# Kernel optimization log

Hardware: AMD Instinct MI355X
Metric: run time of the kernel (lower is better)

## Reference

```python
import jax, jax.numpy as jnp
import numpy as np

K = 5  # AUTKC top-K parameter


def setup_inputs() -> dict:
    key = jax.random.key(0)
    k1, k2 = jax.random.split(key)
    B, C = 4096, 32000
    pred = jax.random.normal(k1, (B, C), dtype=jnp.float32)
    y = jax.random.randint(k2, (B,), 0, C, dtype=jnp.int64)
    return {"pred": pred, "y": y, "epoch": 1}


def reference(pred, y, epoch):
    # epoch >= epoch_to_paced (=0), so the main AUTKC branch runs.
    B, C = pred.shape
    # surrogate != 'Hinge' -> softmax over classes
    probs = jax.nn.softmax(pred, axis=-1)                      # [B, C]
    pred_p = probs[jnp.arange(B), y][:, None]                  # [B, 1] positive-class prob
    pos_mask = jnp.arange(C)[None, :] == y[:, None]            # [B, C] boolean one-hot
    # Mask out the positive entry; top_k(K+1) over negatives == sort desc + take K+1.
    neg = jnp.where(pos_mask, -jnp.inf, probs)                 # [B, C]
    top_n, _ = jax.lax.top_k(neg, K + 1)                       # [B, K+1]
    # 'Sq' surrogate: (1 + s_neg - s_pos)^2
    loss = jnp.sum((1.0 + top_n - pred_p) ** 2, axis=-1) / K   # [B]
    return jnp.mean(loss)
```

## Files before the change

### kernel.cpp

```cpp
#include <hip/hip_runtime.h>
#include <math.h>

#define BLOCK 256
#define KTOP 7
#define RBLK 1024

__device__ __forceinline__ void proc4(const float4 v, float& s, float t[KTOP]) {
    float vals[4] = {v.x, v.y, v.z, v.w};
#pragma unroll
    for (int c = 0; c < 4; ++c) {
        const float x = vals[c];
        s += __expf(x);
#pragma unroll
        for (int k = KTOP - 1; k >= 1; --k)
            t[k] = __builtin_amdgcn_fmed3f(t[k - 1], t[k], x);
        t[0] = fmaxf(t[0], x);
    }
}

__global__ __launch_bounds__(BLOCK)
void autkc_row_kernel(const float* __restrict__ pred,
                      const int* __restrict__ y,
                      float* __restrict__ row_loss,
                      int C) {
    const int row = blockIdx.x;
    const int tid = threadIdx.x;
    const float* prow = pred + (size_t)row * (size_t)C;
    const float4* p4 = (const float4*)prow;
    const int nvec = C >> 2;

    const int yy = y[row];
    const float py = prow[yy];

    float t[KTOP];
#pragma unroll
    for (int k = 0; k < KTOP; ++k) t[k] = -INFINITY;
    float s0 = 0.f, s1 = 0.f, s2 = 0.f, s3 = 0.f;

    int i = tid;
    for (; i + 3 * BLOCK < nvec; i += 4 * BLOCK) {
        float4 a = p4[i];
        float4 b = p4[i + BLOCK];
        float4 c = p4[i + 2 * BLOCK];
        float4 d = p4[i + 3 * BLOCK];
        proc4(a, s0, t);
        proc4(b, s1, t);
        proc4(c, s2, t);
        proc4(d, s3, t);
    }
    for (; i < nvec; i += BLOCK) proc4(p4[i], s0, t);
    const float s = (s0 + s1) + (s2 + s3);

    __shared__ float red[BLOCK][9];
#pragma unroll
    for (int k = 0; k < KTOP; ++k) red[tid][k] = t[k];
    red[tid][KTOP] = s;
    __syncthreads();

    for (int half = BLOCK / 2; half >= 1; half >>= 1) {
        if (tid < half) {
            float a[KTOP], b[KTOP];
#pragma unroll
            for (int k = 0; k < KTOP; ++k) {
                a[k] = red[tid][k];
                b[k] = red[tid + half][k];
            }
            float c[KTOP];
#pragma unroll
            for (int k = 0; k < KTOP; ++k) {
                float best = -INFINITY;
#pragma unroll
                for (int m = 0; m <= k + 1; ++m) {
                    const int bi = (k - m) >= 0 ? (k - m) : 0;
                    float av = (m > 0) ? a[m - 1] : INFINITY;
                    float bv = ((k + 1 - m) > 0) ? b[bi] : INFINITY;
                    best = fmaxf(best, fminf(av, bv));
                }
                c[k] = best;
            }
#pragma unroll
            for (int k = 0; k < KTOP; ++k) red[tid][k] = c[k];
            red[tid][KTOP] = red[tid][KTOP] + red[tid + half][KTOP];
        }
        __syncthreads();
    }

    if (tid == 0) {
        float m[KTOP];
#pragma unroll
        for (int k = 0; k < KTOP; ++k) m[k] = red[0][k];
        const float S   = red[0][KTOP];
        const float inv = 1.0f / S;
        const float pp  = __expf(py) * inv;

        int r = KTOP;
#pragma unroll
        for (int k = KTOP - 1; k >= 0; --k)
            if (m[k] == py) r = k;

        float acc = 0.0f;
#pragma unroll
        for (int j = 0; j < 6; ++j) {
            const float nv = (j < r) ? m[j] : m[j + 1];
            const float d  = 1.0f + __expf(nv) * inv - pp;
            acc += d * d;
        }
        row_loss[row] = acc * 0.2f;
    }
}

__global__ __launch_bounds__(RBLK)
void autkc_reduce_kernel(const float* __restrict__ row_loss,
                         float* __restrict__ out, int B) {
    __shared__ float sh[RBLK];
    const int tid = threadIdx.x;
    float s = 0.0f;
    const int n4 = B >> 2;
    const float4* r4 = (const float4*)row_loss;
    for (int i = tid; i < n4; i += RBLK) {
        float4 v = r4[i];
        s += (v.x + v.y) + (v.z + v.w);
    }
    for (int i = (n4 << 2) + tid; i < B; i += RBLK) s += row_loss[i];
    sh[tid] = s;
    __syncthreads();
    for (int half = RBLK / 2; half >= 1; half >>= 1) {
        if (tid < half) sh[tid] += sh[tid + half];
        __syncthreads();
    }
    if (tid == 0) out[0] = sh[0] / (float)B;
}

extern "C" void kernel_launch(void* const* d_in, const int* in_sizes, int n_in,
                              void* d_out, int out_size, void* d_ws, size_t ws_size,
                              hipStream_t stream) {
    const float* pred = (const float*)d_in[0];
    const int*   y    = (const int*)d_in[1];

    const int B = in_sizes[1];
    const int C = in_sizes[0] / B;

    float* row_loss = (float*)d_ws;

    autkc_row_kernel<<<B, BLOCK, 0, stream>>>(pred, y, row_loss, C);
    autkc_reduce_kernel<<<1, RBLK, 0, stream>>>(row_loss, (float*)d_out, B);
}
```

Baseline: 101.1 us.

## Filter top-K candidates by threshold into shared memory instead of per-element insertion

Replaces the per-element 7-deep median insertion network with a threshold filter: values above 3.0 are appended to a shared candidate buffer via shared-memory atomics, and the top-K is then built from those candidates. If the candidate count is below K or overflows the buffer, it falls back to a second pass over the row with the full insertion network. This cuts ALU work in the main streaming loop for standard-normal inputs. It relies on an input-distribution-dependent threshold, uses shared atomics, and adds a second global read when the fallback triggers.

```diff
diff --git a/kernel.cpp b/kernel.cpp
--- a/kernel.cpp
+++ b/kernel.cpp
@@ -4,17 +4,32 @@
 #define BLOCK 256
 #define KTOP 7
 #define RBLK 1024
+#define THR  3.0f
+#define CAP  512
 
-__device__ __forceinline__ void proc4(const float4 v, float& s, float t[KTOP]) {
+__device__ __forceinline__ void insert4(const float4 v, float t[KTOP]) {
+    float vals[4] = {v.x, v.y, v.z, v.w};
+#pragma unroll
+    for (int c = 0; c < 4; ++c) {
+        const float x = vals[c];
+#pragma unroll
+        for (int k = KTOP - 1; k >= 1; --k)
+            t[k] = __builtin_amdgcn_fmed3f(t[k - 1], t[k], x);
+        t[0] = fmaxf(t[0], x);
+    }
+}
+
+__device__ __forceinline__ void fsum4(const float4 v, float& s,
+                                      int* cnt, float* cand) {
     float vals[4] = {v.x, v.y, v.z, v.w};
 #pragma unroll
     for (int c = 0; c < 4; ++c) {
         const float x = vals[c];
         s += __expf(x);
-#pragma unroll
-        for (int k = KTOP - 1; k >= 1; --k)
-            t[k] = __builtin_amdgcn_fmed3f(t[k - 1], t[k], x);
-        t[0] = fmaxf(t[0], x);
+        if (x > THR) {
+            const int idx = atomicAdd(cnt, 1);
+            if (idx < CAP) cand[idx] = x;
+        }
     }
 }
 
@@ -32,9 +47,11 @@
     const int yy = y[row];
     const float py = prow[yy];
 
-    float t[KTOP];
-#pragma unroll
-    for (int k = 0; k < KTOP; ++k) t[k] = -INFINITY;
+    __shared__ int cnt;
+    __shared__ float cand[CAP];
+    if (tid == 0) cnt = 0;
+    __syncthreads();
+
     float s0 = 0.f, s1 = 0.f, s2 = 0.f, s3 = 0.f;
 
     int i = tid;
@@ -43,13 +60,30 @@
         float4 b = p4[i + BLOCK];
         float4 c = p4[i + 2 * BLOCK];
         float4 d = p4[i + 3 * BLOCK];
-        proc4(a, s0, t);
-        proc4(b, s1, t);
-        proc4(c, s2, t);
-        proc4(d, s3, t);
+        fsum4(a, s0, &cnt, cand);
+        fsum4(b, s1, &cnt, cand);
+        fsum4(c, s2, &cnt, cand);
+        fsum4(d, s3, &cnt, cand);
     }
-    for (; i < nvec; i += BLOCK) proc4(p4[i], s0, t);
+    for (; i < nvec; i += BLOCK) fsum4(p4[i], s0, &cnt, cand);
     const float s = (s0 + s1) + (s2 + s3);
+
+    __syncthreads();
+    const int n = cnt;
+
+    float t[KTOP];
+    if (n >= KTOP && n <= CAP) {
+        const float c0 = (tid < n) ? cand[tid] : -INFINITY;
+        const float c1 = (tid + BLOCK < n) ? cand[tid + BLOCK] : -INFINITY;
+        t[0] = fmaxf(c0, c1);
+        t[1] = fminf(c0, c1);
+#pragma unroll
+        for (int k = 2; k < KTOP; ++k) t[k] = -INFINITY;
+    } else {
+#pragma unroll
+        for (int k = 0; k < KTOP; ++k) t[k] = -INFINITY;
+        for (int j = tid; j < nvec; j += BLOCK) insert4(p4[j], t);
+    }
 
     __shared__ float red[BLOCK][9];
 #pragma unroll
```

Result: no change. 100.1 us (median of 2 runs) (-1.0%).
